# Kernel optimization log

Hardware: AMD Instinct MI355X
Metric: run time of the kernel (lower is better)

## Reference

```python
import jax, jax.numpy as jnp
import numpy as np

DIM = 512
HEADS = 8
SCALE = (DIM / HEADS) ** (-0.5)  # = head_dim^-0.5


def setup_inputs() -> dict:
    key = jax.random.key(0)
    kq, kk, kv = jax.random.split(key, 3)
    B, N, D = 4, 2048, DIM
    return {
        "Q": jax.random.normal(kq, (B, N, D), dtype=jnp.float32),
        "K": jax.random.normal(kk, (B, N, D), dtype=jnp.float32),
        "V": jax.random.normal(kv, (B, N, D), dtype=jnp.float32),
    }


def _split_heads(x):
    b, n, hd = x.shape
    d = hd // HEADS
    return x.reshape(b, n, HEADS, d).transpose(0, 2, 1, 3)  # [b,h,n,d]


def reference(Q, K, V):
    q = _split_heads(Q)
    k = _split_heads(K)
    v = _split_heads(V)
    dots = jnp.einsum('bhid,bhjd->bhij', q, k) * SCALE
    attn = jax.nn.softmax(dots, axis=-1)
    out = jnp.einsum('bhij,bhjd->bhid', attn, v)
    b, h, n, d = out.shape
    return out.transpose(0, 2, 1, 3).reshape(b, n, h * d)
```

## Files before the change

kernel.cpp:

```cpp
#include <hip/hip_runtime.h>

typedef _Float16 half4 __attribute__((ext_vector_type(4)));
typedef _Float16 half8 __attribute__((ext_vector_type(8)));
typedef float floatx4 __attribute__((ext_vector_type(4)));

constexpr int NSEQ = 2048;
constexpr int NDIM = 512;
constexpr int DH   = 64;
constexpr float SCALE = 0.125f;
constexpr float SCALE_L2E = 0.125f * 1.44269504088896340736f;

constexpr int KB9 = 32;
constexpr int NT9 = NSEQ / KB9;
constexpr int KB = 64;
constexpr int NT = NSEQ / KB;

#if __has_builtin(__builtin_amdgcn_exp2f)
__device__ __forceinline__ float fast_exp2(float x) { return __builtin_amdgcn_exp2f(x); }
#else
__device__ __forceinline__ float fast_exp2(float x) {
    float r; asm("v_exp_f32 %0, %1\n\ts_nop 1" : "=v"(r) : "v"(x)); return r;
}
#endif

__global__ __launch_bounds__(256) void mha_prep9(const float* __restrict__ K,
                                                 const float* __restrict__ V,
                                                 _Float16* __restrict__ Kh,
                                                 _Float16* __restrict__ Vh)
{
    const int bid = blockIdx.x;
    const int isV = bid >> 11;
    const int t   = bid & 2047;
    const int kt  = t & 63, bh = t >> 6;
    const int h = bh & 7, b = bh >> 3;
    const int n0 = kt * KB9;
    _Float16* dst = (isV ? Vh : Kh) + (size_t)(bh * 64 + kt) * 2048;

    const int tid = threadIdx.x;
    const int f = tid >> 6, l = tid & 63, lr = l & 15, lg = l >> 4;
    half8 w;
    if (!isV) {
        const int row = n0 + (f >> 1) * 16 + lr;
        const int c0  = (f & 1) * 32 + lg * 8;
        const float* src = K + ((size_t)b * NSEQ + row) * NDIM + h * DH + c0;
        floatx4 x0 = *(const floatx4*)src;
        floatx4 x1 = *(const floatx4*)(src + 4);
        #pragma unroll
        for (int j = 0; j < 4; ++j) { w[j] = (_Float16)x0[j]; w[4 + j] = (_Float16)x1[j]; }
    } else {
        const int d  = f * 16 + lr;
        const int k0 = lg * 4;
        const float* src = V + ((size_t)(b * NSEQ + n0 + k0)) * NDIM + h * DH + d;
        #pragma unroll
        for (int j = 0; j < 4; ++j) {
            w[j]     = (_Float16)src[(size_t)j * NDIM];
            w[4 + j] = (_Float16)src[(size_t)(16 + j) * NDIM];
        }
    }
    *(half8*)(dst + (size_t)tid * 8) = w;
}

__launch_bounds__(128, 3)
__global__ void mha_fwd12(const float* __restrict__ Q,
                          const _Float16* __restrict__ Kh,
                          const _Float16* __restrict__ Vh,
                          float* __restrict__ O)
{
    __shared__ float mrg[34][64];

    const int tid = threadIdx.x, wave = tid >> 6, lane = tid & 63;
    const int lr = lane & 15, lg = lane >> 4;

    const int bid = blockIdx.x;
    const int bh  = (bid & 7) + 8 * (bid >> 9);
    const int qw  = (bid >> 3) & 63;
    const int h = bh & 7, b = bh >> 3;
    const int qrow0 = qw * 32;

    half8 aq[2][2];
    #pragma unroll
    for (int qs = 0; qs < 2; ++qs) {
        const float* qp = Q + ((size_t)b * NSEQ + qrow0 + qs * 16 + lr) * NDIM + h * DH;
        #pragma unroll
        for (int c = 0; c < 2; ++c) {
            floatx4 x0 = *(const floatx4*)(qp + c * 32 + lg * 8);
            floatx4 x1 = *(const floatx4*)(qp + c * 32 + lg * 8 + 4);
            #pragma unroll
            for (int j = 0; j < 4; ++j) {
                aq[qs][c][j]     = (_Float16)(x0[j] * SCALE_L2E);
                aq[qs][c][4 + j] = (_Float16)(x1[j] * SCALE_L2E);
            }
        }
    }

    const char* kbase = (const char*)Kh + (size_t)bh * 64 * 4096 + lane * 16;
    const char* vbase = (const char*)Vh + (size_t)bh * 64 * 4096 + lane * 16;

    floatx4 accT[4][2];
    floatx4 accL[2];
    #pragma unroll
    for (int dt = 0; dt < 4; ++dt)
        #pragma unroll
        for (int qs = 0; qs < 2; ++qs) accT[dt][qs] = (floatx4){0.f, 0.f, 0.f, 0.f};
    #pragma unroll
    for (int qs = 0; qs < 2; ++qs) accL[qs] = (floatx4){0.f, 0.f, 0.f, 0.f};
    const half8 ones8 = {(_Float16)1.f, (_Float16)1.f, (_Float16)1.f, (_Float16)1.f,
                         (_Float16)1.f, (_Float16)1.f, (_Float16)1.f, (_Float16)1.f};

    const int kt0 = wave * (NT9 / 2);

    for (int it = 0; it < NT9 / 2; ++it) {
        const char* kp = kbase + (size_t)(kt0 + it) * 4096;
        const char* vp = vbase + (size_t)(kt0 + it) * 4096;
        half8 kf0 = *(const half8*)(kp);
        half8 kf1 = *(const half8*)(kp + 1024);
        half8 kf2 = *(const half8*)(kp + 2048);
        half8 kf3 = *(const half8*)(kp + 3072);
        half8 vf0 = *(const half8*)(vp);
        half8 vf1 = *(const half8*)(vp + 1024);
        half8 vf2 = *(const half8*)(vp + 2048);
        half8 vf3 = *(const half8*)(vp + 3072);

        #pragma unroll
        for (int qs = 0; qs < 2; ++qs) {
            floatx4 s0 = (floatx4){0.f, 0.f, 0.f, 0.f};
            s0 = __builtin_amdgcn_mfma_f32_16x16x32_f16(kf0, aq[qs][0], s0, 0, 0, 0);
            s0 = __builtin_amdgcn_mfma_f32_16x16x32_f16(kf1, aq[qs][1], s0, 0, 0, 0);
            floatx4 s1 = (floatx4){0.f, 0.f, 0.f, 0.f};
            s1 = __builtin_amdgcn_mfma_f32_16x16x32_f16(kf2, aq[qs][0], s1, 0, 0, 0);
            s1 = __builtin_amdgcn_mfma_f32_16x16x32_f16(kf3, aq[qs][1], s1, 0, 0, 0);

            union { unsigned int u[4]; half8 h; } pw;
            {
                const float e0 = fast_exp2(s0[0]);
                const float e1 = fast_exp2(s0[1]);
                const float e2 = fast_exp2(s0[2]);
                const float e3 = fast_exp2(s0[3]);
                pw.u[0] = __builtin_bit_cast(unsigned int, __builtin_amdgcn_cvt_pkrtz(e0, e1));
                pw.u[1] = __builtin_bit_cast(unsigned int, __builtin_amdgcn_cvt_pkrtz(e2, e3));
            }
            {
                const float e0 = fast_exp2(s1[0]);
                const float e1 = fast_exp2(s1[1]);
                const float e2 = fast_exp2(s1[2]);
                const float e3 = fast_exp2(s1[3]);
                pw.u[2] = __builtin_bit_cast(unsigned int, __builtin_amdgcn_cvt_pkrtz(e0, e1));
                pw.u[3] = __builtin_bit_cast(unsigned int, __builtin_amdgcn_cvt_pkrtz(e2, e3));
            }
            const half8 pb8 = pw.h;

            __builtin_amdgcn_s_setprio(1);
            accL[qs] = __builtin_amdgcn_mfma_f32_16x16x32_f16(ones8, pb8, accL[qs], 0, 0, 0);
            accT[0][qs] = __builtin_amdgcn_mfma_f32_16x16x32_f16(vf0, pb8, accT[0][qs], 0, 0, 0);
            accT[1][qs] = __builtin_amdgcn_mfma_f32_16x16x32_f16(vf1, pb8, accT[1][qs], 0, 0, 0);
            accT[2][qs] = __builtin_amdgcn_mfma_f32_16x16x32_f16(vf2, pb8, accT[2][qs], 0, 0, 0);
            accT[3][qs] = __builtin_amdgcn_mfma_f32_16x16x32_f16(vf3, pb8, accT[3][qs], 0, 0, 0);
            __builtin_amdgcn_s_setprio(0);
        }
    }

    __syncthreads();
    if (wave == 1) {
        #pragma unroll
        for (int dt = 0; dt < 4; ++dt)
            #pragma unroll
            for (int qs = 0; qs < 2; ++qs)
                #pragma unroll
                for (int r = 0; r < 4; ++r)
                    mrg[dt * 8 + qs * 4 + r][lane] = accT[dt][qs][r];
        #pragma unroll
        for (int qs = 0; qs < 2; ++qs) mrg[32 + qs][lane] = accL[qs][0];
    }
    __syncthreads();
    if (wave == 0) {
        #pragma unroll
        for (int qs = 0; qs < 2; ++qs) {
            const float inv = 1.0f / (accL[qs][0] + mrg[32 + qs][lane]);
            float* op = O + ((size_t)b * NSEQ + qrow0 + qs * 16 + lr) * NDIM + h * DH;
            #pragma unroll
            for (int dt = 0; dt < 4; ++dt) {
                floatx4 o;
                #pragma unroll
                for (int r = 0; r < 4; ++r)
                    o[r] = (accT[dt][qs][r] + mrg[dt * 8 + qs * 4 + r][lane]) * inv;
                *(floatx4*)(op + dt * 16 + lg * 4) = o;
            }
        }
    }
}

constexpr int QB2 = 64;
constexpr int LDK = DH + 8;
constexpr int LDV = KB + 8;

__launch_bounds__(256, 4)
__global__ void mha_fwd2(const float* __restrict__ Q,
                         const float* __restrict__ K,
                         const float* __restrict__ V,
                         float* __restrict__ O)
{
    __shared__ _Float16 sK[2][KB * LDK];
    __shared__ _Float16 sVT[2][DH * LDV];

    const int tid = threadIdx.x, wave = tid >> 6, lane = tid & 63;
    const int lr = lane & 15, lg = lane >> 4;
    const int bid = blockIdx.x;
    const int qt = bid & 31, bh = bid >> 5;
    const int h = bh & 7, b = bh >> 3;
    const int qrow0 = qt * QB2 + wave * 16;

    half8 aq[2];
    {
        const float* qp = Q + ((size_t)b * NSEQ + qrow0 + lr) * NDIM + h * DH;
        #pragma unroll
        for (int c = 0; c < 2; ++c) {
            floatx4 x0 = *(const floatx4*)(qp + c * 32 + lg * 8);
            floatx4 x1 = *(const floatx4*)(qp + c * 32 + lg * 8 + 4);
            #pragma unroll
            for (int j = 0; j < 4; ++j) {
                aq[c][j] = (_Float16)(x0[j] * SCALE);
                aq[c][4 + j] = (_Float16)(x1[j] * SCALE);
            }
        }
    }
    const int jk = tid >> 2, ck = (tid & 3) * 16;
    const int jv = (tid & 15) * 4, cv = (tid >> 4) * 4;
    const float* kbase = K + (size_t)b * NSEQ * NDIM + h * DH;
    const float* vbase = V + (size_t)b * NSEQ * NDIM + h * DH;

    floatx4 rk[4], rv[4];
    auto LOAD = [&](int kt) {
        const float* ks = kbase + (size_t)(kt * KB + jk) * NDIM + ck;
        #pragma unroll
        for (int q4 = 0; q4 < 4; ++q4) rk[q4] = *(const floatx4*)(ks + q4 * 4);
        const float* vs = vbase + (size_t)(kt * KB + jv) * NDIM + cv;
        #pragma unroll
        for (int i = 0; i < 4; ++i) rv[i] = *(const floatx4*)(vs + (size_t)i * NDIM);
    };
    auto WRITE = [&](int buf) {
        #pragma unroll
        for (int q4 = 0; q4 < 4; ++q4) {
            half4 w = { (_Float16)rk[q4][0], (_Float16)rk[q4][1],
                        (_Float16)rk[q4][2], (_Float16)rk[q4][3] };
            *(half4*)&sK[buf][jk * LDK + ck + q4 * 4] = w;
        }
        #pragma unroll
        for (int cc = 0; cc < 4; ++cc) {
            half4 w = { (_Float16)rv[0][cc], (_Float16)rv[1][cc],
                        (_Float16)rv[2][cc], (_Float16)rv[3][cc] };
            *(half4*)&sVT[buf][(cv + cc) * LDV + jv] = w;
        }
    };

    floatx4 accT[4];
    #pragma unroll
    for (int t = 0; t < 4; ++t) accT[t] = (floatx4){0.f, 0.f, 0.f, 0.f};
    float m_run = -1e30f, l_run = 0.f;

    LOAD(0);
    #pragma unroll 2
    for (int kt = 0; kt < NT; ++kt) {
        const int buf = kt & 1;
        WRITE(buf);
        if (kt + 1 < NT) LOAD(kt + 1);
        __syncthreads();

        floatx4 s[4];
        #pragma unroll
        for (int t = 0; t < 4; ++t) {
            half8 bk0 = *(const half8*)&sK[buf][(t * 16 + lr) * LDK + lg * 8];
            half8 bk1 = *(const half8*)&sK[buf][(t * 16 + lr) * LDK + 32 + lg * 8];
            floatx4 z = (floatx4){0.f, 0.f, 0.f, 0.f};
            z = __builtin_amdgcn_mfma_f32_16x16x32_f16(bk0, aq[0], z, 0, 0, 0);
            z = __builtin_amdgcn_mfma_f32_16x16x32_f16(bk1, aq[1], z, 0, 0, 0);
            s[t] = z;
        }
        float lm = s[0][0];
        #pragma unroll
        for (int t = 0; t < 4; ++t)
            #pragma unroll
            for (int r = 0; r < 4; ++r) lm = fmaxf(lm, s[t][r]);
        lm = fmaxf(lm, __shfl_xor(lm, 16, 64));
        lm = fmaxf(lm, __shfl_xor(lm, 32, 64));
        const float mn = fmaxf(m_run, lm);
        const float f = __expf(m_run - mn);
        m_run = mn;
        #pragma unroll
        for (int t = 0; t < 4; ++t)
            #pragma unroll
            for (int r = 0; r < 4; ++r) s[t][r] = __expf(s[t][r] - mn);
        float ls = 0.f;
        #pragma unroll
        for (int t = 0; t < 4; ++t) ls += (s[t][0] + s[t][1]) + (s[t][2] + s[t][3]);
        ls += __shfl_xor(ls, 16, 64);
        ls += __shfl_xor(ls, 32, 64);
        l_run = l_run * f + ls;
        #pragma unroll
        for (int dt = 0; dt < 4; ++dt)
            #pragma unroll
            for (int r = 0; r < 4; ++r) accT[dt][r] *= f;

        half4 pb[4];
        #pragma unroll
        for (int t = 0; t < 4; ++t) {
            half4 w = { (_Float16)s[t][0], (_Float16)s[t][1],
                        (_Float16)s[t][2], (_Float16)s[t][3] };
            pb[t] = w;
        }
        #pragma unroll
        for (int dt = 0; dt < 4; ++dt) {
            #pragma unroll
            for (int t = 0; t < 4; ++t) {
                half4 va = *(const half4*)&sVT[buf][(dt * 16 + lr) * LDV + t * 16 + lg * 4];
                accT[dt] = __builtin_amdgcn_mfma_f32_16x16x16f16(va, pb[t], accT[dt], 0, 0, 0);
            }
        }
    }
    const float inv = 1.0f / l_run;
    float* op = O + ((size_t)b * NSEQ + qrow0 + lr) * NDIM + h * DH;
    #pragma unroll
    for (int dt = 0; dt < 4; ++dt) {
        floatx4 o;
        #pragma unroll
        for (int r = 0; r < 4; ++r) o[r] = accT[dt][r] * inv;
        *(floatx4*)(op + dt * 16 + lg * 4) = o;
    }
}

extern "C" void kernel_launch(void* const* d_in, const int* in_sizes, int n_in,
                              void* d_out, int out_size, void* d_ws, size_t ws_size,
                              hipStream_t stream) {
    const float* Q = (const float*)d_in[0];
    const float* K = (const float*)d_in[1];
    const float* V = (const float*)d_in[2];
    float* O = (float*)d_out;

    const size_t need = (size_t)2 * 32 * 64 * 2048 * sizeof(_Float16);
    if (ws_size >= need) {
        _Float16* Kh = (_Float16*)d_ws;
        _Float16* Vh = Kh + (size_t)32 * 64 * 2048;
        hipLaunchKernelGGL(mha_prep9, dim3(4096), dim3(256), 0, stream, K, V, Kh, Vh);
        hipLaunchKernelGGL(mha_fwd12, dim3(2048), dim3(128), 0, stream, Q, Kh, Vh, O);
    } else {
        hipLaunchKernelGGL(mha_fwd2, dim3(1024), dim3(256), 0, stream, Q, K, V, O);
    }
}
```

Baseline: 59.62 us.

## Double the block to four waves and prefetch the next K tile in registers

The attention kernel now runs 256-thread blocks, each covering two 32-row query groups with the key range split in half, so each block holds four waves and the grid is halved. Inside the key loop the K fragments for the next tile are loaded into a second register set while the current tile is computed, unrolled by two with ping-pong buffers. The aim is to hide global load latency and let paired waves in one block share K/V lines in cache. The cost is more registers per wave, which could reduce occupancy under the launch bound of 3 blocks of 256 threads.

```diff
diff --git a/kernel.cpp b/kernel.cpp
--- a/kernel.cpp
+++ b/kernel.cpp
@@ -60,22 +60,23 @@
     *(half8*)(dst + (size_t)tid * 8) = w;
 }
 
-__launch_bounds__(128, 3)
-__global__ void mha_fwd12(const float* __restrict__ Q,
+__launch_bounds__(256, 3)
+__global__ void mha_fwd13(const float* __restrict__ Q,
                           const _Float16* __restrict__ Kh,
                           const _Float16* __restrict__ Vh,
                           float* __restrict__ O)
 {
-    __shared__ float mrg[34][64];
+    __shared__ float mrg[2][34][64];
 
     const int tid = threadIdx.x, wave = tid >> 6, lane = tid & 63;
+    const int qgrp = wave & 1, khalf = wave >> 1;
     const int lr = lane & 15, lg = lane >> 4;
 
     const int bid = blockIdx.x;
-    const int bh  = (bid & 7) + 8 * (bid >> 9);
-    const int qw  = (bid >> 3) & 63;
+    const int bh  = (bid & 7) + 8 * (bid >> 8);
+    const int qw  = (bid >> 3) & 31;
     const int h = bh & 7, b = bh >> 3;
-    const int qrow0 = qw * 32;
+    const int qrow0 = qw * 64 + qgrp * 32;
 
     half8 aq[2][2];
     #pragma unroll
@@ -107,28 +108,36 @@
     const half8 ones8 = {(_Float16)1.f, (_Float16)1.f, (_Float16)1.f, (_Float16)1.f,
                          (_Float16)1.f, (_Float16)1.f, (_Float16)1.f, (_Float16)1.f};
 
-    const int kt0 = wave * (NT9 / 2);
-
-    for (int it = 0; it < NT9 / 2; ++it) {
-        const char* kp = kbase + (size_t)(kt0 + it) * 4096;
-        const char* vp = vbase + (size_t)(kt0 + it) * 4096;
-        half8 kf0 = *(const half8*)(kp);
-        half8 kf1 = *(const half8*)(kp + 1024);
-        half8 kf2 = *(const half8*)(kp + 2048);
-        half8 kf3 = *(const half8*)(kp + 3072);
+    half8 kA[4], kB[4];
+
+    const int kt0 = khalf * (NT9 / 2);
+    const int ktL = kt0 + NT9 / 2 - 1;
+
+    auto LK = [&](int kt, half8* d) {
+        const char* p = kbase + (size_t)kt * 4096;
+        d[0] = *(const half8*)(p);
+        d[1] = *(const half8*)(p + 1024);
+        d[2] = *(const half8*)(p + 2048);
+        d[3] = *(const half8*)(p + 3072);
+    };
+
+    auto BODY = [&](int kt, half8* kC, half8* kN) {
+        const char* vp = vbase + (size_t)kt * 4096;
         half8 vf0 = *(const half8*)(vp);
         half8 vf1 = *(const half8*)(vp + 1024);
         half8 vf2 = *(const half8*)(vp + 2048);
         half8 vf3 = *(const half8*)(vp + 3072);
+        const int ktn = (kt < ktL) ? kt + 1 : kt;
+        LK(ktn, kN);
 
         #pragma unroll
         for (int qs = 0; qs < 2; ++qs) {
             floatx4 s0 = (floatx4){0.f, 0.f, 0.f, 0.f};
-            s0 = __builtin_amdgcn_mfma_f32_16x16x32_f16(kf0, aq[qs][0], s0, 0, 0, 0);
-            s0 = __builtin_amdgcn_mfma_f32_16x16x32_f16(kf1, aq[qs][1], s0, 0, 0, 0);
+            s0 = __builtin_amdgcn_mfma_f32_16x16x32_f16(kC[0], aq[qs][0], s0, 0, 0, 0);
+            s0 = __builtin_amdgcn_mfma_f32_16x16x32_f16(kC[1], aq[qs][1], s0, 0, 0, 0);
             floatx4 s1 = (floatx4){0.f, 0.f, 0.f, 0.f};
-            s1 = __builtin_amdgcn_mfma_f32_16x16x32_f16(kf2, aq[qs][0], s1, 0, 0, 0);
-            s1 = __builtin_amdgcn_mfma_f32_16x16x32_f16(kf3, aq[qs][1], s1, 0, 0, 0);
+            s1 = __builtin_amdgcn_mfma_f32_16x16x32_f16(kC[2], aq[qs][0], s1, 0, 0, 0);
+            s1 = __builtin_amdgcn_mfma_f32_16x16x32_f16(kC[3], aq[qs][1], s1, 0, 0, 0);
 
             union { unsigned int u[4]; half8 h; } pw;
             {
@@ -157,32 +166,40 @@
             accT[3][qs] = __builtin_amdgcn_mfma_f32_16x16x32_f16(vf3, pb8, accT[3][qs], 0, 0, 0);
             __builtin_amdgcn_s_setprio(0);
         }
+    };
+
+    LK(kt0, kA);
+    for (int it = 0; it < NT9 / 2; it += 2) {
+        BODY(kt0 + it,     kA, kB);
+        BODY(kt0 + it + 1, kB, kA);
     }
 
     __syncthreads();
-    if (wave == 1) {
+    if (khalf == 1) {
+        float (*m)[64] = mrg[qgrp];
         #pragma unroll
         for (int dt = 0; dt < 4; ++dt)
             #pragma unroll
             for (int qs = 0; qs < 2; ++qs)
                 #pragma unroll
                 for (int r = 0; r < 4; ++r)
-                    mrg[dt * 8 + qs * 4 + r][lane] = accT[dt][qs][r];
-        #pragma unroll
-        for (int qs = 0; qs < 2; ++qs) mrg[32 + qs][lane] = accL[qs][0];
+                    m[dt * 8 + qs * 4 + r][lane] = accT[dt][qs][r];
+        #pragma unroll
+        for (int qs = 0; qs < 2; ++qs) m[32 + qs][lane] = accL[qs][0];
     }
     __syncthreads();
-    if (wave == 0) {
+    if (khalf == 0) {
+        float (*m)[64] = mrg[qgrp];
         #pragma unroll
         for (int qs = 0; qs < 2; ++qs) {
-            const float inv = 1.0f / (accL[qs][0] + mrg[32 + qs][lane]);
+            const float inv = 1.0f / (accL[qs][0] + m[32 + qs][lane]);
             float* op = O + ((size_t)b * NSEQ + qrow0 + qs * 16 + lr) * NDIM + h * DH;
             #pragma unroll
             for (int dt = 0; dt < 4; ++dt) {
                 floatx4 o;
                 #pragma unroll
                 for (int r = 0; r < 4; ++r)
-                    o[r] = (accT[dt][qs][r] + mrg[dt * 8 + qs * 4 + r][lane]) * inv;
+                    o[r] = (accT[dt][qs][r] + m[dt * 8 + qs * 4 + r][lane]) * inv;
                 *(floatx4*)(op + dt * 16 + lg * 4) = o;
             }
         }
@@ -340,7 +357,7 @@
         _Float16* Kh = (_Float16*)d_ws;
         _Float16* Vh = Kh + (size_t)32 * 64 * 2048;
         hipLaunchKernelGGL(mha_prep9, dim3(4096), dim3(256), 0, stream, K, V, Kh, Vh);
-        hipLaunchKernelGGL(mha_fwd12, dim3(2048), dim3(128), 0, stream, Q, Kh, Vh, O);
+        hipLaunchKernelGGL(mha_fwd13, dim3(1024), dim3(256), 0, stream, Q, Kh, Vh, O);
     } else {
         hipLaunchKernelGGL(mha_fwd2, dim3(1024), dim3(256), 0, stream, Q, K, V, O);
     }
```

New measurement: 59.73 us. Within noise of the previous version (+0.2%).
